# Kernel optimization log

Measured on AMD Instinct MI355X. Metric: run time of the kernel, lower is better.

## Reference

```python
import jax, jax.numpy as jnp
import numpy as np

D_MODEL = 1024
NUM_HEADS = 16


def setup_inputs() -> dict:
    key = jax.random.key(0)
    ks = jax.random.split(key, 5)
    B, T, d = 2, 2048, D_MODEL
    s = 1.0 / np.sqrt(d)
    return {
        "x": jax.random.normal(ks[0], (B, T, d), dtype=jnp.float32),
        "W_kqv": jax.random.normal(ks[1], (d, 3 * d), dtype=jnp.float32) * s,
        "b_kqv": jax.random.normal(ks[2], (3 * d,), dtype=jnp.float32) * 0.02,
        "W_o": jax.random.normal(ks[3], (d, d), dtype=jnp.float32) * s,
        "b_o": jax.random.normal(ks[4], (d,), dtype=jnp.float32) * 0.02,
    }


def reference(x, W_kqv, b_kqv, W_o, b_o):
    B, T, d = x.shape
    H = NUM_HEADS
    dk = d // H
    kqv = x @ W_kqv + b_kqv                      # [B, T, 3d]
    # source splits as contiguous chunks in order K, Q, V
    K, Q, V = jnp.split(kqv, 3, axis=-1)
    # [B, T, d] -> [B, H, T, dk]
    to_heads = lambda t: t.reshape(B, T, H, dk).transpose(0, 2, 1, 3)
    K, Q, V = to_heads(K), to_heads(Q), to_heads(V)
    scores = jnp.einsum("bhtd,bhsd->bhts", Q, K)  # [B, H, T, T]
    causal = jnp.triu(jnp.ones((T, T), dtype=bool), k=1)
    scores = jnp.where(causal, -jnp.inf, scores)
    attn = jax.nn.softmax(scores / jnp.sqrt(jnp.asarray(dk, x.dtype)), axis=-1)
    out = jnp.einsum("bhts,bhsd->bhtd", attn, V)  # [B, H, T, dk]
    out = out.transpose(0, 2, 1, 3).reshape(B, T, d)
    return out @ W_o + b_o
```

## Files before the change

kernel.cpp:

```cpp
#include <hip/hip_runtime.h>
#include <hip/hip_bf16.h>
#include <stdint.h>
#include <math.h>

using bf16x8 = __attribute__((ext_vector_type(8))) short;
using f32x4  = __attribute__((ext_vector_type(4))) float;
using f32x16 = __attribute__((ext_vector_type(16))) float;

#define NHEAD  16
#define DK     64
#define TSEQ   2048
#define DMODEL 1024
#define MTOT   4096

#define QSCALE 0.18033688011112042f

static __device__ __forceinline__ ushort f2bf(float f) {
  union { float f; uint32_t u; } v; v.f = f;
  return (ushort)((v.u + 0x7FFFu + ((v.u >> 16) & 1u)) >> 16);
}

static __device__ __forceinline__ float bf2f(ushort u) {
  union { uint32_t u; float f; } v; v.u = ((uint32_t)u) << 16;
  return v.f;
}

static __device__ __forceinline__ uint32_t cvtpk_bf16(float lo, float hi) {
  uint32_t r;
  asm("v_cvt_pk_bf16_f32 %0, %1, %2" : "=v"(r) : "v"(lo), "v"(hi));
  return r;
}

static __device__ __forceinline__ void gload_lds16(const ushort* g, ushort* l) {
  typedef __attribute__((address_space(1))) const uint32_t gu32;
  typedef __attribute__((address_space(3))) uint32_t lu32;
  __builtin_amdgcn_global_load_lds((gu32*)g, (lu32*)l, 16, 0, 0);
}

__global__ void cvt_bf16_kernel(const float* __restrict__ in, ushort* __restrict__ out, int n) {
  int i = (blockIdx.x * 256 + threadIdx.x) * 8;
  const int stride = gridDim.x * 256 * 8;
  for (; i < n; i += stride) {
    const float4* p = (const float4*)(in + i);
    float4 a = p[0], b = p[1];
    bf16x8 v;
    v[0]=(short)f2bf(a.x); v[1]=(short)f2bf(a.y); v[2]=(short)f2bf(a.z); v[3]=(short)f2bf(a.w);
    v[4]=(short)f2bf(b.x); v[5]=(short)f2bf(b.y); v[6]=(short)f2bf(b.z); v[7]=(short)f2bf(b.w);
    *(bf16x8*)(out + i) = v;
  }
}

__global__ __launch_bounds__(256) void transpose_cvt2_kernel(const float* __restrict__ W1,
                                                             ushort* __restrict__ Wt1,
                                                             const float* __restrict__ W2,
                                                             ushort* __restrict__ Wt2) {
  __shared__ ushort tl[64][66];
  const int bx = blockIdx.x;
  const float* W; ushort* Wt; int N, n0;
  if (bx < 48) { W = W1; Wt = Wt1; N = 3072; n0 = bx * 64; }
  else         { W = W2; Wt = Wt2; N = 1024; n0 = (bx - 48) * 64; }
  const int k0 = blockIdx.y * 64;
  const int c = threadIdx.x & 63, r0 = threadIdx.x >> 6;
#pragma unroll
  for (int i = 0; i < 64; i += 4)
    tl[i + r0][c] = f2bf(W[(size_t)(k0 + i + r0) * N + n0 + c]);
  __syncthreads();
#pragma unroll
  for (int i = 0; i < 64; i += 4)
    Wt[(size_t)(n0 + i + r0) * 1024 + k0 + c] = tl[c][i + r0];
}

__global__ __launch_bounds__(256) void transpose_v_kernel(const ushort* __restrict__ V,
                                                          ushort* __restrict__ Vt) {
  __shared__ ushort tl[64][66];
  const int bh = blockIdx.y, t0 = blockIdx.x * 64;
  const int c = threadIdx.x & 63, r0 = threadIdx.x >> 6;
  const ushort* Vb = V + (size_t)bh * TSEQ * DK;
  ushort* Vtb = Vt + (size_t)bh * DK * TSEQ;
#pragma unroll
  for (int i = 0; i < 64; i += 4)
    tl[i + r0][c] = Vb[(size_t)(t0 + i + r0) * DK + c];
  __syncthreads();
#pragma unroll
  for (int i = 0; i < 64; i += 4)
    Vtb[(size_t)(i + r0) * TSEQ + t0 + c] = tl[c][i + r0];
}

template <int MODE>
__global__ __launch_bounds__(256, 3)
void gemm_bt_kernel(const ushort* __restrict__ A, const ushort* __restrict__ Bt,
                    const float* __restrict__ bias,
                    ushort* __restrict__ oK, ushort* __restrict__ oQ, ushort* __restrict__ oV,
                    float* __restrict__ oF, int N, int K) {
  __shared__ ushort As[2][128 * 32];
  __shared__ ushort Bs[2][128 * 32];
  const int tid = threadIdx.x;
  const int w = tid >> 6, lane = tid & 63;
  const int m0 = blockIdx.y * 128, n0 = blockIdx.x * 128;
  const int wr = (w >> 1) * 64, wc = (w & 1) * 64;

  const int e0 = ((w * 2 + 0) * 64 + lane) * 8;
  const int e1 = ((w * 2 + 1) * 64 + lane) * 8;
  const ushort* pA0 = A  + (size_t)(m0 + (e0 >> 5)) * K + (e0 & 31);
  const ushort* pA1 = A  + (size_t)(m0 + (e1 >> 5)) * K + (e1 & 31);
  const ushort* pB0 = Bt + (size_t)(n0 + (e0 >> 5)) * K + (e0 & 31);
  const ushort* pB1 = Bt + (size_t)(n0 + (e1 >> 5)) * K + (e1 & 31);

  f32x4 acc[4][4];
#pragma unroll
  for (int i = 0; i < 4; i++)
#pragma unroll
    for (int j = 0; j < 4; j++) acc[i][j] = (f32x4){0.f, 0.f, 0.f, 0.f};

  const int aro = (wr + (lane & 15)) * 32 + (lane >> 4) * 8;
  const int bro = (wc + (lane & 15)) * 32 + (lane >> 4) * 8;

  gload_lds16(pA0, &As[0][e0]);
  gload_lds16(pA1, &As[0][e1]);
  gload_lds16(pB0, &Bs[0][e0]);
  gload_lds16(pB1, &Bs[0][e1]);
  asm volatile("s_waitcnt vmcnt(0)" ::: "memory");
  __builtin_amdgcn_s_barrier();

  for (int k0 = 0; k0 < K; k0 += 32) {
    const int cur = (k0 >> 5) & 1;
    if (k0 + 32 < K) {
      const int nb = cur ^ 1, kn = k0 + 32;
      gload_lds16(pA0 + kn, &As[nb][e0]);
      gload_lds16(pA1 + kn, &As[nb][e1]);
      gload_lds16(pB0 + kn, &Bs[nb][e0]);
      gload_lds16(pB1 + kn, &Bs[nb][e1]);
    }
    bf16x8 af[4], bfr[4];
#pragma unroll
    for (int i = 0; i < 4; i++) af[i]  = *(const bf16x8*)&As[cur][aro + i * 16 * 32];
#pragma unroll
    for (int j = 0; j < 4; j++) bfr[j] = *(const bf16x8*)&Bs[cur][bro + j * 16 * 32];
    __builtin_amdgcn_s_setprio(1);
#pragma unroll
    for (int i = 0; i < 4; i++)
#pragma unroll
      for (int j = 0; j < 4; j++)
        acc[i][j] = __builtin_amdgcn_mfma_f32_16x16x32_bf16(af[i], bfr[j], acc[i][j], 0, 0, 0);
    __builtin_amdgcn_s_setprio(0);
    asm volatile("s_waitcnt vmcnt(0)" ::: "memory");
    __builtin_amdgcn_s_barrier();
  }

  const int rbase = m0 + wr + (lane >> 4) * 4;
  const int cbase = n0 + wc + (lane & 15);
#pragma unroll
  for (int i = 0; i < 4; i++) {
#pragma unroll
    for (int j = 0; j < 4; j++) {
      const int gn = cbase + j * 16;
      const float bv = bias[gn];
#pragma unroll
      for (int jj = 0; jj < 4; jj++) {
        const int gm = rbase + i * 16 + jj;
        float val = acc[i][j][jj] + bv;
        if (MODE == 0) {
          const int sel = gn >> 10, cc = gn & 1023;
          const int hh = cc >> 6, dd = cc & 63;
          const int bbx = gm >> 11, t = gm & 2047;
          if (sel == 1) val *= QSCALE;
          ushort* dst = (sel == 0) ? oK : (sel == 1) ? oQ : oV;
          dst[((size_t)((bbx * NHEAD + hh) * TSEQ + t)) * DK + dd] = f2bf(val);
        } else {
          oF[(size_t)gm * N + gn] = val;
        }
      }
    }
  }
}

__global__ __launch_bounds__(256, 5)
void attn_kernel(const ushort* __restrict__ Qb, const ushort* __restrict__ Kb,
                 const ushort* __restrict__ Vtb, ushort* __restrict__ Opart,
                 float2* __restrict__ mlbuf) {
  __shared__ ushort Ks[2][64 * 64];
  __shared__ ushort Vs[2][64 * 64];

  const int bid = blockIdx.x;
  const int xcd = bid & 7, i = bid >> 3;
  const int bh = xcd + 8 * (i / 40);
  const int jj = 39 - (i % 40);
  int qi, p;
  if (jj < 4)       { qi = jj;                 p = 0; }
  else if (jj < 12) { int t = jj - 4;  qi = 4  + (t >> 1); p = t & 1; }
  else if (jj < 24) { int t = jj - 12; qi = 8  + t / 3;    p = t % 3; }
  else              { int t = jj - 24; qi = 12 + (t >> 2); p = t & 3; }

  const int q0 = qi * 128;
  const int tid = threadIdx.x, w = tid >> 6, lane = tid & 63;
  const int l31 = lane & 31, h = lane >> 5;
  const int qrow = q0 + w * 32 + l31;

  const int t_begin = p * 8;
  const int ntp = min(t_begin + 8, 2 * qi + 2) - t_begin;

  const ushort* Qp = Qb + ((size_t)bh * TSEQ + qrow) * DK;
  bf16x8 qf[4];
#pragma unroll
  for (int c = 0; c < 4; c++)
    qf[c] = *(const bf16x8*)(Qp + c * 16 + h * 8);

  f32x16 oacc0, oacc1;
#pragma unroll
  for (int r = 0; r < 16; r++) { oacc0[r] = 0.f; oacc1[r] = 0.f; }
  float mrun = -INFINITY, lrun = 0.f;

  const int Bl0 = w * 128 + lane, Bl1 = Bl0 + 64;
  const int sr0 = Bl0 >> 3, sc0 = ((Bl0 & 7) ^ (sr0 & 7)) * 8;
  const int sr1 = Bl1 >> 3, sc1 = ((Bl1 & 7) ^ (sr1 & 7)) * 8;
  const ushort* Kp0 = Kb  + (size_t)bh * TSEQ * DK + sr0 * DK + sc0;
  const ushort* Kp1 = Kb  + (size_t)bh * TSEQ * DK + sr1 * DK + sc1;
  const ushort* Vp0 = Vtb + (size_t)bh * DK * TSEQ + sr0 * TSEQ + sc0;
  const ushort* Vp1 = Vtb + (size_t)bh * DK * TSEQ + sr1 * TSEQ + sc1;

  {
    const int s0 = t_begin * 64;
    gload_lds16(Kp0 + s0 * DK, &Ks[0][Bl0 * 8]);
    gload_lds16(Kp1 + s0 * DK, &Ks[0][Bl1 * 8]);
    gload_lds16(Vp0 + s0, &Vs[0][Bl0 * 8]);
    gload_lds16(Vp1 + s0, &Vs[0][Bl1 * 8]);
  }
  asm volatile("s_waitcnt vmcnt(0)" ::: "memory");
  __builtin_amdgcn_s_barrier();

  for (int tt = 0; tt < ntp; tt++) {
    const int s0 = (t_begin + tt) * 64, cur = tt & 1;

    if (tt + 1 < ntp) {
      const int sn = (t_begin + tt + 1) * 64, nb = cur ^ 1;
      gload_lds16(Kp0 + sn * DK, &Ks[nb][Bl0 * 8]);
      gload_lds16(Kp1 + sn * DK, &Ks[nb][Bl1 * 8]);
      gload_lds16(Vp0 + sn, &Vs[nb][Bl0 * 8]);
      gload_lds16(Vp1 + sn, &Vs[nb][Bl1 * 8]);
    }

    const bool active = (s0 <= q0 + w * 32 + 31);
    if (active) {
      f32x16 ps0, ps1;
#pragma unroll
      for (int r = 0; r < 16; r++) { ps0[r] = 0.f; ps1[r] = 0.f; }
      const char* Kbase = (const char*)&Ks[cur][0];
      __builtin_amdgcn_s_setprio(1);
#pragma unroll
      for (int c = 0; c < 4; c++) {
        const int r0 = l31, r1 = 32 + l31;
        bf16x8 kf0 = *(const bf16x8*)(Kbase + r0 * 128 + ((c * 32 + h * 16) ^ ((r0 & 7) << 4)));
        bf16x8 kf1 = *(const bf16x8*)(Kbase + r1 * 128 + ((c * 32 + h * 16) ^ ((r1 & 7) << 4)));
        ps0 = __builtin_amdgcn_mfma_f32_32x32x16_bf16(kf0, qf[c], ps0, 0, 0, 0);
        ps1 = __builtin_amdgcn_mfma_f32_32x32x16_bf16(kf1, qf[c], ps1, 0, 0, 0);
      }
      __builtin_amdgcn_s_setprio(0);

      if (s0 + 63 > q0 + w * 32) {
#pragma unroll
        for (int r = 0; r < 16; r++) {
          const int kv0 = s0 + (r & 3) + 8 * (r >> 2) + 4 * h;
          if (kv0 > qrow)      ps0[r] = -INFINITY;
          if (kv0 + 32 > qrow) ps1[r] = -INFINITY;
        }
      }

      float pm = ps0[0];
#pragma unroll
      for (int r = 1; r < 16; r++) pm = fmaxf(pm, ps0[r]);
#pragma unroll
      for (int r = 0; r < 16; r++) pm = fmaxf(pm, ps1[r]);
      pm = fmaxf(pm, __shfl_xor(pm, 32));

      if (!__all(pm <= mrun + 8.0f)) {
        const float nm = fmaxf(mrun, pm);
        const float scl = exp2f(mrun - nm);
        lrun *= scl;
#pragma unroll
        for (int r = 0; r < 16; r++) { oacc0[r] *= scl; oacc1[r] *= scl; }
        mrun = nm;
      }

#pragma unroll
      for (int r = 0; r < 16; r++) ps0[r] = exp2f(ps0[r] - mrun);
#pragma unroll
      for (int r = 0; r < 16; r++) ps1[r] = exp2f(ps1[r] - mrun);
      float rs = 0.f;
#pragma unroll
      for (int r = 0; r < 16; r++) rs += ps0[r] + ps1[r];
      rs += __shfl_xor(rs, 32);
      lrun += rs;

      uint32_t w0[2][4], w1[2][4];
#pragma unroll
      for (int a = 0; a < 4; a++) {
        w0[0][a] = cvtpk_bf16(ps0[4 * a + 0], ps0[4 * a + 1]);
        w1[0][a] = cvtpk_bf16(ps0[4 * a + 2], ps0[4 * a + 3]);
        w0[1][a] = cvtpk_bf16(ps1[4 * a + 0], ps1[4 * a + 1]);
        w1[1][a] = cvtpk_bf16(ps1[4 * a + 2], ps1[4 * a + 3]);
      }

      const char* Vbase = (const char*)&Vs[cur][0];
#pragma unroll
      for (int s = 0; s < 2; s++) {
#pragma unroll
        for (int u = 0; u < 2; u++) {
          const int t = 2 * s + u;
          const uint32_t sw0 = h ? w0[s][2 * u] : w0[s][2 * u + 1];
          const uint32_t sw1 = h ? w1[s][2 * u] : w1[s][2 * u + 1];
          const uint32_t rx0 = (uint32_t)__shfl_xor((int)sw0, 32);
          const uint32_t rx1 = (uint32_t)__shfl_xor((int)sw1, 32);
          int4 pw;
          pw.x = h ? (int)rx0 : (int)w0[s][2 * u];
          pw.y = h ? (int)rx1 : (int)w1[s][2 * u];
          pw.z = h ? (int)w0[s][2 * u + 1] : (int)rx0;
          pw.w = h ? (int)w1[s][2 * u + 1] : (int)rx1;
          const bf16x8 pf = __builtin_bit_cast(bf16x8, pw);

          const int vr0 = l31, vr1 = 32 + l31;
          bf16x8 vf0 = *(const bf16x8*)(Vbase + vr0 * 128 + ((t * 32 + h * 16) ^ ((vr0 & 7) << 4)));
          bf16x8 vf1 = *(const bf16x8*)(Vbase + vr1 * 128 + ((t * 32 + h * 16) ^ ((vr1 & 7) << 4)));
          __builtin_amdgcn_s_setprio(1);
          oacc0 = __builtin_amdgcn_mfma_f32_32x32x16_bf16(vf0, pf, oacc0, 0, 0, 0);
          oacc1 = __builtin_amdgcn_mfma_f32_32x32x16_bf16(vf1, pf, oacc1, 0, 0, 0);
          __builtin_amdgcn_s_setprio(0);
        }
      }
    }

    asm volatile("s_waitcnt vmcnt(0)" ::: "memory");
    __builtin_amdgcn_s_barrier();
  }

  const int partIdx = (bh * 16 + qi) * 4 + p;
  const size_t rowslot = (size_t)partIdx * 128 + (qrow & 127);
  ushort* orow = Opart + rowslot * 64;
#pragma unroll
  for (int r = 0; r < 16; r += 2) {
    const int d0 = (r & 3) + 8 * (r >> 2) + 4 * h;
    const uint32_t v0 = (uint32_t)f2bf(oacc0[r]) | ((uint32_t)f2bf(oacc0[r + 1]) << 16);
    const uint32_t v1 = (uint32_t)f2bf(oacc1[r]) | ((uint32_t)f2bf(oacc1[r + 1]) << 16);
    *(uint32_t*)(orow + d0)      = v0;
    *(uint32_t*)(orow + 32 + d0) = v1;
  }
  if (h == 0) mlbuf[rowslot] = make_float2(mrun, lrun);
}

__global__ __launch_bounds__(256) void combine_kernel(const ushort* __restrict__ Opart,
                                                      const float2* __restrict__ mlbuf,
                                                      ushort* __restrict__ AO) {
  const int gid = blockIdx.x * 4 + (threadIdx.x >> 6);
  const int lane = threadIdx.x & 63;
  const int bh = gid >> 11, q = gid & 2047;
  const int qi = q >> 7, np = (qi >> 2) + 1;
  const size_t base = ((size_t)(bh * 16 + qi) * 4) * 128 + (q & 127);

  float M = -INFINITY;
  for (int p = 0; p < np; p++) M = fmaxf(M, mlbuf[base + (size_t)p * 128].x);
  float den = 0.f, acc = 0.f;
  for (int p = 0; p < np; p++) {
    const float2 ml = mlbuf[base + (size_t)p * 128];
    const float wp = exp2f(ml.x - M);
    den += wp * ml.y;
    acc += wp * bf2f(Opart[(base + (size_t)p * 128) * 64 + lane]);
  }
  const float val = acc / den;
  const int bb = bh >> 4, hd = bh & 15;
  AO[((size_t)bb * TSEQ + q) * DMODEL + hd * DK + lane] = f2bf(val);
}

extern "C" void kernel_launch(void* const* d_in, const int* in_sizes, int n_in,
                              void* d_out, int out_size, void* d_ws, size_t ws_size,
                              hipStream_t stream) {
  (void)in_sizes; (void)n_in; (void)out_size; (void)ws_size;
  const float* x    = (const float*)d_in[0];
  const float* Wkqv = (const float*)d_in[1];
  const float* bkqv = (const float*)d_in[2];
  const float* Wo   = (const float*)d_in[3];
  const float* bo   = (const float*)d_in[4];
  float* out = (float*)d_out;

  char* ws = (char*)d_ws;
  const size_t MB = 1024 * 1024;
  ushort* x_bf   = (ushort*)(ws + 0);
  ushort* wkqv_t = (ushort*)(ws + 8 * MB);
  ushort* wo_t   = (ushort*)(ws + 14 * MB);
  ushort* Kbuf   = (ushort*)(ws + 16 * MB);
  ushort* Qbuf   = (ushort*)(ws + 24 * MB);
  ushort* Vbuf   = (ushort*)(ws + 32 * MB);
  ushort* Vtbuf  = (ushort*)(ws + 40 * MB);
  ushort* AObuf  = (ushort*)(ws + 48 * MB);
  ushort* Opart  = (ushort*)(ws + 56 * MB);
  float2* mlbuf  = (float2*)(ws + 88 * MB);

  cvt_bf16_kernel<<<2048, 256, 0, stream>>>(x, x_bf, MTOT * DMODEL);
  transpose_cvt2_kernel<<<dim3(64, 16), 256, 0, stream>>>(Wkqv, wkqv_t, Wo, wo_t);
  gemm_bt_kernel<0><<<dim3(3072 / 128, 4096 / 128), 256, 0, stream>>>(
      x_bf, wkqv_t, bkqv, Kbuf, Qbuf, Vbuf, nullptr, 3072, 1024);
  transpose_v_kernel<<<dim3(TSEQ / 64, 32), 256, 0, stream>>>(Vbuf, Vtbuf);
  attn_kernel<<<1280, 256, 0, stream>>>(Qbuf, Kbuf, Vtbuf, Opart, mlbuf);
  combine_kernel<<<16384, 256, 0, stream>>>(Opart, mlbuf, AObuf);
  gemm_bt_kernel<1><<<dim3(1024 / 128, 4096 / 128), 256, 0, stream>>>(
      AObuf, wo_t, bo, nullptr, nullptr, nullptr, out, 1024, 1024);
}
```

Before: 229.0 us.

## Fuse prep kernels, write transposed V from GEMM, fold combine into attention

Merges the x conversion and weight transpose into a single prep launch. The QKV GEMM epilogue now writes V directly in transposed layout, which removes the separate V transpose kernel. The split-KV combine moves into the attention kernel: a per-tile atomic counter lets the last finishing block merge the partial results. The max and sum reductions use tree form, and attention occupancy drops from 5 to 4 blocks. These changes cut launches and intermediate round-trips, at the cost of atomics, a memset, and extra register pressure in the attention kernel.

Result: slower. 311.2 us (+35.9%).

```diff
diff --git a/kernel.cpp b/kernel.cpp
--- a/kernel.cpp
+++ b/kernel.cpp
@@ -37,30 +37,31 @@
   __builtin_amdgcn_global_load_lds((gu32*)g, (lu32*)l, 16, 0, 0);
 }
 
-__global__ void cvt_bf16_kernel(const float* __restrict__ in, ushort* __restrict__ out, int n) {
-  int i = (blockIdx.x * 256 + threadIdx.x) * 8;
-  const int stride = gridDim.x * 256 * 8;
-  for (; i < n; i += stride) {
-    const float4* p = (const float4*)(in + i);
-    float4 a = p[0], b = p[1];
+__global__ __launch_bounds__(256) void prep_kernel(const float* __restrict__ x,
+                                                   ushort* __restrict__ x_bf,
+                                                   const float* __restrict__ W1,
+                                                   ushort* __restrict__ Wt1,
+                                                   const float* __restrict__ W2,
+                                                   ushort* __restrict__ Wt2) {
+  __shared__ ushort tl[64][66];
+  const int b = blockIdx.x, tid = threadIdx.x;
+  if (b < 2048) {
+    const int i = (b * 256 + tid) * 8;
+    const float4* p = (const float4*)(x + i);
+    float4 a = p[0], bb = p[1];
     bf16x8 v;
     v[0]=(short)f2bf(a.x); v[1]=(short)f2bf(a.y); v[2]=(short)f2bf(a.z); v[3]=(short)f2bf(a.w);
-    v[4]=(short)f2bf(b.x); v[5]=(short)f2bf(b.y); v[6]=(short)f2bf(b.z); v[7]=(short)f2bf(b.w);
-    *(bf16x8*)(out + i) = v;
-  }
-}
-
-__global__ __launch_bounds__(256) void transpose_cvt2_kernel(const float* __restrict__ W1,
-                                                             ushort* __restrict__ Wt1,
-                                                             const float* __restrict__ W2,
-                                                             ushort* __restrict__ Wt2) {
-  __shared__ ushort tl[64][66];
-  const int bx = blockIdx.x;
+    v[4]=(short)f2bf(bb.x); v[5]=(short)f2bf(bb.y); v[6]=(short)f2bf(bb.z); v[7]=(short)f2bf(bb.w);
+    *(bf16x8*)(x_bf + i) = v;
+    return;
+  }
+  const int b2 = b - 2048;
+  const int bx = b2 & 63, by = b2 >> 6;
   const float* W; ushort* Wt; int N, n0;
   if (bx < 48) { W = W1; Wt = Wt1; N = 3072; n0 = bx * 64; }
   else         { W = W2; Wt = Wt2; N = 1024; n0 = (bx - 48) * 64; }
-  const int k0 = blockIdx.y * 64;
-  const int c = threadIdx.x & 63, r0 = threadIdx.x >> 6;
+  const int k0 = by * 64;
+  const int c = tid & 63, r0 = tid >> 6;
 #pragma unroll
   for (int i = 0; i < 64; i += 4)
     tl[i + r0][c] = f2bf(W[(size_t)(k0 + i + r0) * N + n0 + c]);
@@ -68,29 +69,13 @@
 #pragma unroll
   for (int i = 0; i < 64; i += 4)
     Wt[(size_t)(n0 + i + r0) * 1024 + k0 + c] = tl[c][i + r0];
-}
-
-__global__ __launch_bounds__(256) void transpose_v_kernel(const ushort* __restrict__ V,
-                                                          ushort* __restrict__ Vt) {
-  __shared__ ushort tl[64][66];
-  const int bh = blockIdx.y, t0 = blockIdx.x * 64;
-  const int c = threadIdx.x & 63, r0 = threadIdx.x >> 6;
-  const ushort* Vb = V + (size_t)bh * TSEQ * DK;
-  ushort* Vtb = Vt + (size_t)bh * DK * TSEQ;
-#pragma unroll
-  for (int i = 0; i < 64; i += 4)
-    tl[i + r0][c] = Vb[(size_t)(t0 + i + r0) * DK + c];
-  __syncthreads();
-#pragma unroll
-  for (int i = 0; i < 64; i += 4)
-    Vtb[(size_t)(i + r0) * TSEQ + t0 + c] = tl[c][i + r0];
 }
 
 template <int MODE>
 __global__ __launch_bounds__(256, 3)
 void gemm_bt_kernel(const ushort* __restrict__ A, const ushort* __restrict__ Bt,
                     const float* __restrict__ bias,
-                    ushort* __restrict__ oK, ushort* __restrict__ oQ, ushort* __restrict__ oV,
+                    ushort* __restrict__ oK, ushort* __restrict__ oQ, ushort* __restrict__ oVt,
                     float* __restrict__ oF, int N, int K) {
   __shared__ ushort As[2][128 * 32];
   __shared__ ushort Bs[2][128 * 32];
@@ -155,31 +140,43 @@
     for (int j = 0; j < 4; j++) {
       const int gn = cbase + j * 16;
       const float bv = bias[gn];
-#pragma unroll
-      for (int jj = 0; jj < 4; jj++) {
-        const int gm = rbase + i * 16 + jj;
-        float val = acc[i][j][jj] + bv;
-        if (MODE == 0) {
-          const int sel = gn >> 10, cc = gn & 1023;
-          const int hh = cc >> 6, dd = cc & 63;
-          const int bbx = gm >> 11, t = gm & 2047;
-          if (sel == 1) val *= QSCALE;
-          ushort* dst = (sel == 0) ? oK : (sel == 1) ? oQ : oV;
-          dst[((size_t)((bbx * NHEAD + hh) * TSEQ + t)) * DK + dd] = f2bf(val);
+      if (MODE == 0) {
+        const int sel = gn >> 10, cc = gn & 1023;
+        const int hh = cc >> 6, dd = cc & 63;
+        const int gm0 = rbase + i * 16;
+        const int bbx = gm0 >> 11, t0 = gm0 & 2047;
+        const int bh = bbx * NHEAD + hh;
+        if (sel == 2) {
+          const uint32_t lo = (uint32_t)f2bf(acc[i][j][0] + bv) |
+                              ((uint32_t)f2bf(acc[i][j][1] + bv) << 16);
+          const uint32_t hi = (uint32_t)f2bf(acc[i][j][2] + bv) |
+                              ((uint32_t)f2bf(acc[i][j][3] + bv) << 16);
+          uint2 pk; pk.x = lo; pk.y = hi;
+          *(uint2*)(oVt + ((size_t)bh * DK + dd) * TSEQ + t0) = pk;
         } else {
-          oF[(size_t)gm * N + gn] = val;
+          ushort* dst = (sel == 0) ? oK : oQ;
+          const float sc = (sel == 1) ? QSCALE : 1.0f;
+#pragma unroll
+          for (int jj = 0; jj < 4; jj++)
+            dst[((size_t)bh * TSEQ + t0 + jj) * DK + dd] = f2bf((acc[i][j][jj] + bv) * sc);
         }
-      }
-    }
-  }
-}
-
-__global__ __launch_bounds__(256, 5)
+      } else {
+#pragma unroll
+        for (int jj = 0; jj < 4; jj++)
+          oF[(size_t)(rbase + i * 16 + jj) * N + gn] = acc[i][j][jj] + bv;
+      }
+    }
+  }
+}
+
+__global__ __launch_bounds__(256, 4)
 void attn_kernel(const ushort* __restrict__ Qb, const ushort* __restrict__ Kb,
                  const ushort* __restrict__ Vtb, ushort* __restrict__ Opart,
-                 float2* __restrict__ mlbuf) {
+                 float2* __restrict__ mlbuf, ushort* __restrict__ AO,
+                 int* __restrict__ cnt) {
   __shared__ ushort Ks[2][64 * 64];
   __shared__ ushort Vs[2][64 * 64];
+  __shared__ int lastFlag;
 
   const int bid = blockIdx.x;
   const int xcd = bid & 7, i = bid >> 3;
@@ -195,6 +192,7 @@
   const int tid = threadIdx.x, w = tid >> 6, lane = tid & 63;
   const int l31 = lane & 31, h = lane >> 5;
   const int qrow = q0 + w * 32 + l31;
+  const int np = (qi >> 2) + 1;
 
   const int t_begin = p * 8;
   const int ntp = min(t_begin + 8, 2 * qi + 2) - t_begin;
@@ -265,12 +263,15 @@
         }
       }
 
-      float pm = ps0[0];
-#pragma unroll
-      for (int r = 1; r < 16; r++) pm = fmaxf(pm, ps0[r]);
-#pragma unroll
-      for (int r = 0; r < 16; r++) pm = fmaxf(pm, ps1[r]);
-      pm = fmaxf(pm, __shfl_xor(pm, 32));
+      float tm[8];
+#pragma unroll
+      for (int r = 0; r < 8; r++)
+        tm[r] = fmaxf(fmaxf(ps0[r], ps0[r + 8]), fmaxf(ps1[r], ps1[r + 8]));
+#pragma unroll
+      for (int s = 4; s > 0; s >>= 1)
+#pragma unroll
+        for (int r = 0; r < s; r++) tm[r] = fmaxf(tm[r], tm[r + s]);
+      float pm = fmaxf(tm[0], __shfl_xor(tm[0], 32));
 
       if (!__all(pm <= mrun + 8.0f)) {
         const float nm = fmaxf(mrun, pm);
@@ -285,11 +286,15 @@
       for (int r = 0; r < 16; r++) ps0[r] = exp2f(ps0[r] - mrun);
 #pragma unroll
       for (int r = 0; r < 16; r++) ps1[r] = exp2f(ps1[r] - mrun);
-      float rs = 0.f;
-#pragma unroll
-      for (int r = 0; r < 16; r++) rs += ps0[r] + ps1[r];
-      rs += __shfl_xor(rs, 32);
-      lrun += rs;
+      float ts[8];
+#pragma unroll
+      for (int r = 0; r < 8; r++)
+        ts[r] = (ps0[r] + ps0[r + 8]) + (ps1[r] + ps1[r + 8]);
+#pragma unroll
+      for (int s = 4; s > 0; s >>= 1)
+#pragma unroll
+        for (int r = 0; r < s; r++) ts[r] += ts[r + s];
+      lrun += ts[0] + __shfl_xor(ts[0], 32);
 
       uint32_t w0[2][4], w1[2][4];
 #pragma unroll
@@ -344,29 +349,40 @@
     *(uint32_t*)(orow + 32 + d0) = v1;
   }
   if (h == 0) mlbuf[rowslot] = make_float2(mrun, lrun);
-}
-
-__global__ __launch_bounds__(256) void combine_kernel(const ushort* __restrict__ Opart,
-                                                      const float2* __restrict__ mlbuf,
-                                                      ushort* __restrict__ AO) {
-  const int gid = blockIdx.x * 4 + (threadIdx.x >> 6);
-  const int lane = threadIdx.x & 63;
-  const int bh = gid >> 11, q = gid & 2047;
-  const int qi = q >> 7, np = (qi >> 2) + 1;
-  const size_t base = ((size_t)(bh * 16 + qi) * 4) * 128 + (q & 127);
-
-  float M = -INFINITY;
-  for (int p = 0; p < np; p++) M = fmaxf(M, mlbuf[base + (size_t)p * 128].x);
-  float den = 0.f, acc = 0.f;
-  for (int p = 0; p < np; p++) {
-    const float2 ml = mlbuf[base + (size_t)p * 128];
-    const float wp = exp2f(ml.x - M);
-    den += wp * ml.y;
-    acc += wp * bf2f(Opart[(base + (size_t)p * 128) * 64 + lane]);
-  }
-  const float val = acc / den;
-  const int bb = bh >> 4, hd = bh & 15;
-  AO[((size_t)bb * TSEQ + q) * DMODEL + hd * DK + lane] = f2bf(val);
+
+  __syncthreads();
+  if (tid == 0) {
+    __threadfence();
+    lastFlag = (atomicAdd(&cnt[bh * 16 + qi], 1) == np - 1);
+  }
+  __syncthreads();
+  if (lastFlag) {
+    __threadfence();
+    const int row = tid >> 1, dh = (tid & 1) * 32;
+    const size_t base = (size_t)((bh * 16 + qi) * 4) * 128 + row;
+    float M = -INFINITY;
+    for (int pp = 0; pp < np; pp++) M = fmaxf(M, mlbuf[base + (size_t)pp * 128].x);
+    float den = 0.f, accd[32];
+#pragma unroll
+    for (int d = 0; d < 32; d++) accd[d] = 0.f;
+    for (int pp = 0; pp < np; pp++) {
+      const float2 ml = mlbuf[base + (size_t)pp * 128];
+      const float wp = exp2f(ml.x - M);
+      den += wp * ml.y;
+      const ushort* src = Opart + (base + (size_t)pp * 128) * 64 + dh;
+#pragma unroll
+      for (int d = 0; d < 32; d++) accd[d] += wp * bf2f(src[d]);
+    }
+    const float inv = 1.f / den;
+    const int bb = bh >> 4, hd = bh & 15;
+    ushort* dst = AO + ((size_t)bb * TSEQ + q0 + row) * DMODEL + hd * DK + dh;
+#pragma unroll
+    for (int d = 0; d < 32; d += 2) {
+      const uint32_t pk = (uint32_t)f2bf(accd[d] * inv) |
+                          ((uint32_t)f2bf(accd[d + 1] * inv) << 16);
+      *(uint32_t*)(dst + d) = pk;
+    }
+  }
 }
 
 extern "C" void kernel_launch(void* const* d_in, const int* in_sizes, int n_in,
@@ -387,19 +403,17 @@
   ushort* wo_t   = (ushort*)(ws + 14 * MB);
   ushort* Kbuf   = (ushort*)(ws + 16 * MB);
   ushort* Qbuf   = (ushort*)(ws + 24 * MB);
-  ushort* Vbuf   = (ushort*)(ws + 32 * MB);
-  ushort* Vtbuf  = (ushort*)(ws + 40 * MB);
+  ushort* Vtbuf  = (ushort*)(ws + 32 * MB);
   ushort* AObuf  = (ushort*)(ws + 48 * MB);
   ushort* Opart  = (ushort*)(ws + 56 * MB);
   float2* mlbuf  = (float2*)(ws + 88 * MB);
-
-  cvt_bf16_kernel<<<2048, 256, 0, stream>>>(x, x_bf, MTOT * DMODEL);
-  transpose_cvt2_kernel<<<dim3(64, 16), 256, 0, stream>>>(Wkqv, wkqv_t, Wo, wo_t);
+  int*    cnt    = (int*)   (ws + 90 * MB);
+
+  hipMemsetAsync(cnt, 0, 32 * 16 * sizeof(int), stream);
+  prep_kernel<<<3072, 256, 0, stream>>>(x, x_bf, Wkqv, wkqv_t, Wo, wo_t);
   gemm_bt_kernel<0><<<dim3(3072 / 128, 4096 / 128), 256, 0, stream>>>(
-      x_bf, wkqv_t, bkqv, Kbuf, Qbuf, Vbuf, nullptr, 3072, 1024);
-  transpose_v_kernel<<<dim3(TSEQ / 64, 32), 256, 0, stream>>>(Vbuf, Vtbuf);
-  attn_kernel<<<1280, 256, 0, stream>>>(Qbuf, Kbuf, Vtbuf, Opart, mlbuf);
-  combine_kernel<<<16384, 256, 0, stream>>>(Opart, mlbuf, AObuf);
+      x_bf, wkqv_t, bkqv, Kbuf, Qbuf, Vtbuf, nullptr, 3072, 1024);
+  attn_kernel<<<1280, 256, 0, stream>>>(Qbuf, Kbuf, Vtbuf, Opart, mlbuf, AObuf, cnt);
   gemm_bt_kernel<1><<<dim3(1024 / 128, 4096 / 128), 256, 0, stream>>>(
       AObuf, wo_t, bo, nullptr, nullptr, nullptr, out, 1024, 1024);
 }
```
